# Performance work log

Measured on AMD Instinct MI355X. Metric: run time of the kernel, lower is better.

Reference implementation:

```python
import jax, jax.numpy as jnp
import numpy as np

B, T, N, D = 2, 16, 512, 256
HID, HEADS = 256, 8
HD = HID // HEADS // 2  # 16
SCALE = HD ** -0.5
LAMBDA_INIT = 0.8 - 0.6 * float(np.exp(-0.3 * (2 - 1)))  # layer_idx = 2
LN_EPS = 1e-5


def setup_inputs() -> dict:
    key = jax.random.key(0)
    ks = jax.random.split(key, 8)
    return {
        "x": jax.random.normal(ks[0], (B, T, N, D), dtype=jnp.float32),
        "Wq": jax.random.normal(ks[1], (D, HID), dtype=jnp.float32) * (D ** -0.5),
        "Wk": jax.random.normal(ks[2], (D, HID), dtype=jnp.float32) * (D ** -0.5),
        "Wv": jax.random.normal(ks[3], (D, HID), dtype=jnp.float32) * (D ** -0.5),
        "lq1": jax.random.normal(ks[4], (HD,), dtype=jnp.float32) * 0.1,
        "lk1": jax.random.normal(ks[5], (HD,), dtype=jnp.float32) * 0.1,
        "lq2": jax.random.normal(ks[6], (HD,), dtype=jnp.float32) * 0.1,
        "lk2": jax.random.normal(ks[7], (HD,), dtype=jnp.float32) * 0.1,
        "ln_gamma": jnp.ones((2 * HD,), dtype=jnp.float32),
        "ln_beta": jnp.zeros((2 * HD,), dtype=jnp.float32),
    }


def _attn_pair(q, k, v1, v2):
    # q,k,v*: [BT, N, H, HD]; shared softmax applied to both value halves
    p = jax.nn.softmax(jnp.einsum('bnhd,bmhd->bhnm', q, k) * SCALE, axis=-1)
    o1 = jnp.einsum('bhnm,bmhd->bnhd', p, v1)
    o2 = jnp.einsum('bhnm,bmhd->bnhd', p, v2)
    return jnp.concatenate([o1, o2], axis=-1)  # [BT, N, H, 2*HD]


def reference(x, Wq, Wk, Wv, lq1, lk1, lq2, lk2, ln_gamma, ln_beta):
    b, t, n, d = x.shape
    # 1x1 Conv2d over channel dim == per-token linear projection
    q = jnp.einsum('btnd,dh->btnh', x, Wq).reshape(b * t, n, HEADS, 2 * HD)
    k = jnp.einsum('btnd,dh->btnh', x, Wk).reshape(b * t, n, HEADS, 2 * HD)
    v = jnp.einsum('btnd,dh->btnh', x, Wv).reshape(b * t, n, HEADS, 2 * HD)
    q1, q2 = jnp.split(q, 2, axis=-1)
    k1, k2 = jnp.split(k, 2, axis=-1)
    v1, v2 = jnp.split(v, 2, axis=-1)
    attn1 = _attn_pair(q1, k1, v1, v2)
    attn2 = _attn_pair(q2, k2, v1, v2)
    lam = jnp.exp(jnp.sum(lq1 * lk1)) - jnp.exp(jnp.sum(lq2 * lk2)) + LAMBDA_INIT
    y = attn1 - lam * attn2  # [BT, N, H, 2*HD]
    mu = jnp.mean(y, axis=-1, keepdims=True)
    var = jnp.mean(jnp.square(y - mu), axis=-1, keepdims=True)
    y = (y - mu) * jax.lax.rsqrt(var + LN_EPS) * ln_gamma + ln_beta
    y = y * (1.0 - LAMBDA_INIT)
    return y.reshape(b, t, n, HEADS * 2 * HD)
```

## Files before the change

kernel.cpp:

```cpp
#include <hip/hip_runtime.h>
#include <cmath>

typedef unsigned short u16;
typedef unsigned int   u32;
typedef __attribute__((ext_vector_type(8)))  short short8;
typedef __attribute__((ext_vector_type(4)))  float f32x4;
typedef __attribute__((ext_vector_type(16))) float f32x16;

constexpr int BT    = 32;
constexpr int NTOK  = 512;
constexpr int DIM   = 256;
constexpr int HID   = 256;
constexpr int M_ROWS = BT * NTOK;
constexpr int HM     = M_ROWS * 32;
constexpr size_t TENS = (size_t)M_ROWS * HID;
constexpr float LAMBDA_INIT  = 0.35550906759096927f;
constexpr float ONE_MINUS_LI = 0.6444909324090307f;
constexpr float LN_EPS = 1e-5f;
constexpr float QSCALE = 0.36067376022224085f;

#define MFMA16(a, b, c) __builtin_amdgcn_mfma_f32_16x16x32_bf16((a), (b), (c), 0, 0, 0)
#define MFMA32(a, b, c) __builtin_amdgcn_mfma_f32_32x32x16_bf16((a), (b), (c), 0, 0, 0)

__device__ __forceinline__ u16 f2bf(float f) {
    u32 u = __float_as_uint(f);
    return (u16)((u + 0x7FFFu + ((u >> 16) & 1u)) >> 16);
}

__device__ __forceinline__ float fexp2(float x) {
#if defined(__has_builtin) && __has_builtin(__builtin_amdgcn_exp2f)
    return __builtin_amdgcn_exp2f(x);
#else
    return exp2f(x);
#endif
}

__device__ __forceinline__ u32 pack_trunc(float a, float b) {
    return __builtin_amdgcn_perm(__float_as_uint(b), __float_as_uint(a), 0x07060302u);
}

__global__ __launch_bounds__(256) void prep_w(const float* __restrict__ Wq,
                                              const float* __restrict__ Wk,
                                              const float* __restrict__ Wv,
                                              u16* __restrict__ Wt) {
    const float* W = (blockIdx.z == 0) ? Wq : (blockIdx.z == 1) ? Wk : Wv;
    u16* dst = Wt + (size_t)blockIdx.z * 65536;
    __shared__ float T[64][65];
    const int k0 = blockIdx.x * 64, n0 = blockIdx.y * 64;
    const int tr = threadIdx.x >> 4;
    const int tc = threadIdx.x & 15;
    #pragma unroll
    for (int i = 0; i < 4; ++i) {
        int row = tr + i * 16;
        float4 v = *(const float4*)&W[(size_t)(k0 + row) * HID + n0 + tc * 4];
        T[row][tc * 4 + 0] = v.x; T[row][tc * 4 + 1] = v.y;
        T[row][tc * 4 + 2] = v.z; T[row][tc * 4 + 3] = v.w;
    }
    __syncthreads();
    #pragma unroll
    for (int i = 0; i < 4; ++i) {
        int n = tr + i * 16;
        int k4 = tc * 4;
        uint2 pk;
        pk.x = (u32)f2bf(T[k4 + 0][n]) | ((u32)f2bf(T[k4 + 1][n]) << 16);
        pk.y = (u32)f2bf(T[k4 + 2][n]) | ((u32)f2bf(T[k4 + 3][n]) << 16);
        *(uint2*)&dst[(size_t)(n0 + n) * DIM + k0 + k4] = pk;
    }
}

__global__ __launch_bounds__(256, 3) void proj_kernel(
    const float* __restrict__ x, const u16* __restrict__ Wt,
    u16* __restrict__ Qh, u16* __restrict__ Kh, u16* __restrict__ Vh)
{
    __shared__ u16 As[64 * 72];
    __shared__ u16 Bs[3][64 * 72];

    const int tid  = threadIdx.x;
    const int n0   = blockIdx.x * 64;
    const int m0   = blockIdx.y * 64;
    const int lane = tid & 63;
    const int wv   = tid >> 6;
    const int q16  = lane & 15;
    const int quad = lane >> 4;
    const int mw   = (wv >> 1) * 32;
    const int nw   = (wv & 1) * 32;

    const int sr = tid >> 2;
    const int sc = (tid & 3) * 16;

    f32x4 acc[3][4];
    #pragma unroll
    for (int z = 0; z < 3; ++z)
        #pragma unroll
        for (int t = 0; t < 4; ++t)
            acc[z][t] = (f32x4){0.f, 0.f, 0.f, 0.f};

    float4 ga[4];
    uint4  gb[3][2];
    {
        const float4* xs = (const float4*)&x[(size_t)(m0 + sr) * DIM + sc];
        ga[0] = xs[0]; ga[1] = xs[1]; ga[2] = xs[2]; ga[3] = xs[3];
        #pragma unroll
        for (int z = 0; z < 3; ++z) {
            const uint4* ws4 = (const uint4*)&Wt[(size_t)z * 65536 + (size_t)(n0 + sr) * DIM + sc];
            gb[z][0] = ws4[0]; gb[z][1] = ws4[1];
        }
    }

    for (int it = 0; it < 4; ++it) {
        {
            uint4 o0, o1;
            o0.x = (u32)f2bf(ga[0].x) | ((u32)f2bf(ga[0].y) << 16);
            o0.y = (u32)f2bf(ga[0].z) | ((u32)f2bf(ga[0].w) << 16);
            o0.z = (u32)f2bf(ga[1].x) | ((u32)f2bf(ga[1].y) << 16);
            o0.w = (u32)f2bf(ga[1].z) | ((u32)f2bf(ga[1].w) << 16);
            o1.x = (u32)f2bf(ga[2].x) | ((u32)f2bf(ga[2].y) << 16);
            o1.y = (u32)f2bf(ga[2].z) | ((u32)f2bf(ga[2].w) << 16);
            o1.z = (u32)f2bf(ga[3].x) | ((u32)f2bf(ga[3].y) << 16);
            o1.w = (u32)f2bf(ga[3].z) | ((u32)f2bf(ga[3].w) << 16);
            *(uint4*)&As[sr * 72 + sc]     = o0;
            *(uint4*)&As[sr * 72 + sc + 8] = o1;
            #pragma unroll
            for (int z = 0; z < 3; ++z) {
                *(uint4*)&Bs[z][sr * 72 + sc]     = gb[z][0];
                *(uint4*)&Bs[z][sr * 72 + sc + 8] = gb[z][1];
            }
        }
        __syncthreads();

        if (it < 3) {
            const int kk = (it + 1) * 64;
            const float4* xs = (const float4*)&x[(size_t)(m0 + sr) * DIM + kk + sc];
            ga[0] = xs[0]; ga[1] = xs[1]; ga[2] = xs[2]; ga[3] = xs[3];
            #pragma unroll
            for (int z = 0; z < 3; ++z) {
                const uint4* ws4 = (const uint4*)&Wt[(size_t)z * 65536 + (size_t)(n0 + sr) * DIM + kk + sc];
                gb[z][0] = ws4[0]; gb[z][1] = ws4[1];
            }
        }

        #pragma unroll
        for (int kc = 0; kc < 2; ++kc) {
            short8 a0 = *(const short8*)&As[(mw +      q16) * 72 + kc * 32 + quad * 8];
            short8 a1 = *(const short8*)&As[(mw + 16 + q16) * 72 + kc * 32 + quad * 8];
            #pragma unroll
            for (int z = 0; z < 3; ++z) {
                short8 b0 = *(const short8*)&Bs[z][(nw +      q16) * 72 + kc * 32 + quad * 8];
                short8 b1 = *(const short8*)&Bs[z][(nw + 16 + q16) * 72 + kc * 32 + quad * 8];
                acc[z][0] = MFMA16(a0, b0, acc[z][0]);
                acc[z][1] = MFMA16(a0, b1, acc[z][1]);
                acc[z][2] = MFMA16(a1, b0, acc[z][2]);
                acc[z][3] = MFMA16(a1, b1, acc[z][3]);
            }
        }
        __syncthreads();
    }

    const int hcol = (n0 + nw) >> 5;
    #pragma unroll
    for (int z = 0; z < 3; ++z) {
        u16* C = (z == 0) ? Qh : (z == 1) ? Kh : Vh;
        u16* base = C + (size_t)hcol * HM;
        const float s = (z == 0) ? QSCALE : 1.0f;
        #pragma unroll
        for (int r = 0; r < 4; ++r) {
            const int row = m0 + mw + quad * 4 + r;
            base[(size_t)row * 32 + q16]              = f2bf(acc[z][0][r] * s);
            base[(size_t)row * 32 + q16 + 16]         = f2bf(acc[z][1][r] * s);
            base[(size_t)(row + 16) * 32 + q16]       = f2bf(acc[z][2][r] * s);
            base[(size_t)(row + 16) * 32 + q16 + 16]  = f2bf(acc[z][3][r] * s);
        }
    }
}

__global__ __launch_bounds__(256, 3) void attn_kernel(
    const u16* __restrict__ Qh, const u16* __restrict__ Kh, const u16* __restrict__ Vh,
    const float* __restrict__ lq1, const float* __restrict__ lk1,
    const float* __restrict__ lq2, const float* __restrict__ lk2,
    const float* __restrict__ gamma, const float* __restrict__ beta,
    float* __restrict__ out)
{
    __shared__ u16 Ks[256 * 40];
    __shared__ u16 Vts[32 * 264];
    __shared__ u16 Pb[4][32 * 40];

    const int qh  = blockIdx.x;
    const int h   = blockIdx.y;
    const int bt  = blockIdx.z;
    const int tid = threadIdx.x;
    const int lane = tid & 63;
    const int wv   = tid >> 6;
    const int l31  = lane & 31;
    const int hi   = lane >> 5;

    float sa = 0.f, sb = 0.f;
    #pragma unroll
    for (int d = 0; d < 16; ++d) { sa += lq1[d] * lk1[d]; sb += lq2[d] * lk2[d]; }
    const float lam = __expf(sa) - __expf(sb) + LAMBDA_INIT;

    const int qbase = bt * NTOK + qh * 128 + wv * 32;
    const u16* qrowp = Qh + (size_t)h * HM + (size_t)(qbase + l31) * 32 + hi * 8;
    const short8 B1 = *(const short8*)qrowp;
    const short8 B2 = *(const short8*)(qrowp + 16);

    const f32x16 z16 = {0.f,0.f,0.f,0.f,0.f,0.f,0.f,0.f,0.f,0.f,0.f,0.f,0.f,0.f,0.f,0.f};
    f32x16 O1 = z16, O2 = z16;
    float l1 = 0.f, l2 = 0.f;
    u16* P = &Pb[wv][0];

    for (int chunk = 0; chunk < 2; ++chunk) {
        if (chunk) __syncthreads();
        {
            const uint4* src = (const uint4*)(Kh + (size_t)h * HM +
                                (size_t)(bt * NTOK + chunk * 256 + tid) * 32);
            uint4* dst = (uint4*)&Ks[tid * 40];
            dst[0] = src[0]; dst[1] = src[1]; dst[2] = src[2]; dst[3] = src[3];
        }
        if (tid < 128) {
            const int j0 = tid * 2;
            const u16* v0 = Vh + (size_t)h * HM + (size_t)(bt * NTOK + chunk * 256 + j0) * 32;
            union U { uint4 q[4]; u32 w[16]; } ra, rb;
            #pragma unroll
            for (int i = 0; i < 4; ++i) {
                ra.q[i] = ((const uint4*)v0)[i];
                rb.q[i] = ((const uint4*)(v0 + 32))[i];
            }
            #pragma unroll
            for (int w = 0; w < 16; ++w) {
                u32 lo = __builtin_amdgcn_perm(rb.w[w], ra.w[w], 0x05040100u);
                u32 hi2 = __builtin_amdgcn_perm(rb.w[w], ra.w[w], 0x07060302u);
                *(u32*)&Vts[(2 * w)     * 264 + j0] = lo;
                *(u32*)&Vts[(2 * w + 1) * 264 + j0] = hi2;
            }
        }
        __syncthreads();

        for (int kc = 0; kc < 8; ++kc) {
            const u16* krow = &Ks[(kc * 32 + l31) * 40 + hi * 8];
            const short8 A1 = *(const short8*)krow;
            const short8 A2 = *(const short8*)(krow + 16);
            const u16* vrow = &Vts[l31 * 264 + kc * 32 + hi * 8];
            const short8 Vt0 = *(const short8*)vrow;
            const short8 Vt1 = *(const short8*)(vrow + 16);

            f32x16 S = MFMA32(A1, B1, z16);
            #pragma unroll
            for (int rg = 0; rg < 4; ++rg) {
                float e0 = fexp2(S[4 * rg + 0]);
                float e1 = fexp2(S[4 * rg + 1]);
                float e2 = fexp2(S[4 * rg + 2]);
                float e3 = fexp2(S[4 * rg + 3]);
                l1 += (e0 + e1) + (e2 + e3);
                uint2 w; w.x = pack_trunc(e0, e1); w.y = pack_trunc(e2, e3);
                *(uint2*)&P[l31 * 40 + rg * 8 + hi * 4] = w;
            }
            {
                const short8 P0  = *(const short8*)&P[l31 * 40 + hi * 8];
                const short8 P1f = *(const short8*)&P[l31 * 40 + 16 + hi * 8];
                O1 = MFMA32(P0,  Vt0, O1);
                O1 = MFMA32(P1f, Vt1, O1);
            }
            S = MFMA32(A2, B2, z16);
            #pragma unroll
            for (int rg = 0; rg < 4; ++rg) {
                float e0 = fexp2(S[4 * rg + 0]);
                float e1 = fexp2(S[4 * rg + 1]);
                float e2 = fexp2(S[4 * rg + 2]);
                float e3 = fexp2(S[4 * rg + 3]);
                l2 += (e0 + e1) + (e2 + e3);
                uint2 w; w.x = pack_trunc(e0, e1); w.y = pack_trunc(e2, e3);
                *(uint2*)&P[l31 * 40 + rg * 8 + hi * 4] = w;
            }
            {
                const short8 P0  = *(const short8*)&P[l31 * 40 + hi * 8];
                const short8 P1f = *(const short8*)&P[l31 * 40 + 16 + hi * 8];
                O2 = MFMA32(P0,  Vt0, O2);
                O2 = MFMA32(P1f, Vt1, O2);
            }
        }
    }

    l1 += __shfl_xor(l1, 32);
    l2 += __shfl_xor(l2, 32);
    const float i1base = 1.0f / l1;
    const float i2base = 1.0f / l2;
    const float g = gamma[l31];
    const float bc = beta[l31];

    #pragma unroll
    for (int r = 0; r < 16; ++r) {
        const int qloc = (r & 3) + 8 * (r >> 2) + 4 * hi;
        const float i1 = __shfl(i1base, qloc);
        const float i2 = __shfl(i2base, qloc);
        float y = O1[r] * i1 - lam * (O2[r] * i2);

        float s  = y;
        float s2 = y * y;
        #pragma unroll
        for (int off = 1; off < 32; off <<= 1) {
            s  += __shfl_xor(s,  off);
            s2 += __shfl_xor(s2, off);
        }
        const float mu   = s * (1.0f / 32.0f);
        const float var  = s2 * (1.0f / 32.0f) - mu * mu;
        const float rstd = rsqrtf(var + LN_EPS);

        const int row = qbase + qloc;
        out[(size_t)row * HID + h * 32 + l31] = ((y - mu) * rstd * g + bc) * ONE_MINUS_LI;
    }
}

extern "C" void kernel_launch(void* const* d_in, const int* in_sizes, int n_in,
                              void* d_out, int out_size, void* d_ws, size_t ws_size,
                              hipStream_t stream) {
    const float* x   = (const float*)d_in[0];
    const float* Wq  = (const float*)d_in[1];
    const float* Wk  = (const float*)d_in[2];
    const float* Wv  = (const float*)d_in[3];
    const float* lq1 = (const float*)d_in[4];
    const float* lk1 = (const float*)d_in[5];
    const float* lq2 = (const float*)d_in[6];
    const float* lk2 = (const float*)d_in[7];
    const float* gam = (const float*)d_in[8];
    const float* bet = (const float*)d_in[9];
    float* out = (float*)d_out;

    u16* ws = (u16*)d_ws;
    u16* Wt = ws;
    u16* Qh = Wt + 3 * 65536;
    u16* Kh = Qh + TENS;
    u16* Vh = Kh + TENS;

    hipLaunchKernelGGL(prep_w, dim3(4, 4, 3), dim3(256), 0, stream, Wq, Wk, Wv, Wt);
    hipLaunchKernelGGL(proj_kernel, dim3(HID / 64, M_ROWS / 64), dim3(256), 0, stream,
                       x, Wt, Qh, Kh, Vh);
    hipLaunchKernelGGL(attn_kernel, dim3(4, 8, 32), dim3(256), 0, stream,
                       Qh, Kh, Vh, lq1, lk1, lq2, lk2, gam, bet, out);
}
```

Before: 157.4 us.

## Interleave dual-softmax MFMAs, re-pad LDS, and vectorize projection stores

The attention inner loop now issues both QK^T MFMAs up front and writes both probability tiles into separate per-wave LDS buffers, so exp work on one half can overlap the other half's matrix ops. K and P LDS rows are re-padded from 40 to 36 elements and read with paired 64-bit loads to change the bank-conflict pattern. The projection kernel swaps its MFMA operands so each lane holds four consecutive output columns, which lets it write packed 8-byte stores instead of scattered 2-byte ones. Occupancy for the projection kernel is raised to 4 blocks per SM, which adds register pressure, and the doubled P buffer increases LDS use.

```diff
diff --git a/kernel.cpp b/kernel.cpp
--- a/kernel.cpp
+++ b/kernel.cpp
@@ -39,6 +39,14 @@
     return __builtin_amdgcn_perm(__float_as_uint(b), __float_as_uint(a), 0x07060302u);
 }
 
+__device__ __forceinline__ short8 ldb64x2(const u16* p) {
+    uint2 a = *(const uint2*)p;
+    uint2 b = *(const uint2*)(p + 4);
+    union { u32 u[4]; short8 s; } x;
+    x.u[0] = a.x; x.u[1] = a.y; x.u[2] = b.x; x.u[3] = b.y;
+    return x.s;
+}
+
 __global__ __launch_bounds__(256) void prep_w(const float* __restrict__ Wq,
                                               const float* __restrict__ Wk,
                                               const float* __restrict__ Wv,
@@ -68,7 +76,7 @@
     }
 }
 
-__global__ __launch_bounds__(256, 3) void proj_kernel(
+__global__ __launch_bounds__(256, 4) void proj_kernel(
     const float* __restrict__ x, const u16* __restrict__ Wt,
     u16* __restrict__ Qh, u16* __restrict__ Kh, u16* __restrict__ Vh)
 {
@@ -147,10 +155,10 @@
             for (int z = 0; z < 3; ++z) {
                 short8 b0 = *(const short8*)&Bs[z][(nw +      q16) * 72 + kc * 32 + quad * 8];
                 short8 b1 = *(const short8*)&Bs[z][(nw + 16 + q16) * 72 + kc * 32 + quad * 8];
-                acc[z][0] = MFMA16(a0, b0, acc[z][0]);
-                acc[z][1] = MFMA16(a0, b1, acc[z][1]);
-                acc[z][2] = MFMA16(a1, b0, acc[z][2]);
-                acc[z][3] = MFMA16(a1, b1, acc[z][3]);
+                acc[z][0] = MFMA16(b0, a0, acc[z][0]);
+                acc[z][1] = MFMA16(b1, a0, acc[z][1]);
+                acc[z][2] = MFMA16(b0, a1, acc[z][2]);
+                acc[z][3] = MFMA16(b1, a1, acc[z][3]);
             }
         }
         __syncthreads();
@@ -163,12 +171,13 @@
         u16* base = C + (size_t)hcol * HM;
         const float s = (z == 0) ? QSCALE : 1.0f;
         #pragma unroll
-        for (int r = 0; r < 4; ++r) {
-            const int row = m0 + mw + quad * 4 + r;
-            base[(size_t)row * 32 + q16]              = f2bf(acc[z][0][r] * s);
-            base[(size_t)row * 32 + q16 + 16]         = f2bf(acc[z][1][r] * s);
-            base[(size_t)(row + 16) * 32 + q16]       = f2bf(acc[z][2][r] * s);
-            base[(size_t)(row + 16) * 32 + q16 + 16]  = f2bf(acc[z][3][r] * s);
+        for (int t = 0; t < 4; ++t) {
+            const int m  = m0 + mw + ((t >> 1) << 4) + q16;
+            const int c0 = ((t & 1) << 4) + quad * 4;
+            uint2 w;
+            w.x = (u32)f2bf(acc[z][t][0] * s) | ((u32)f2bf(acc[z][t][1] * s) << 16);
+            w.y = (u32)f2bf(acc[z][t][2] * s) | ((u32)f2bf(acc[z][t][3] * s) << 16);
+            *(uint2*)&base[(size_t)m * 32 + c0] = w;
         }
     }
 }
@@ -180,9 +189,9 @@
     const float* __restrict__ gamma, const float* __restrict__ beta,
     float* __restrict__ out)
 {
-    __shared__ u16 Ks[256 * 40];
+    __shared__ u16 Ks[256 * 36];
     __shared__ u16 Vts[32 * 264];
-    __shared__ u16 Pb[4][32 * 40];
+    __shared__ u16 Pb[4][2][32 * 36];
 
     const int qh  = blockIdx.x;
     const int h   = blockIdx.y;
@@ -206,15 +215,19 @@
     const f32x16 z16 = {0.f,0.f,0.f,0.f,0.f,0.f,0.f,0.f,0.f,0.f,0.f,0.f,0.f,0.f,0.f,0.f};
     f32x16 O1 = z16, O2 = z16;
     float l1 = 0.f, l2 = 0.f;
-    u16* P = &Pb[wv][0];
+    u16* P1 = &Pb[wv][0][0];
+    u16* P2 = &Pb[wv][1][0];
 
     for (int chunk = 0; chunk < 2; ++chunk) {
         if (chunk) __syncthreads();
         {
             const uint4* src = (const uint4*)(Kh + (size_t)h * HM +
                                 (size_t)(bt * NTOK + chunk * 256 + tid) * 32);
-            uint4* dst = (uint4*)&Ks[tid * 40];
-            dst[0] = src[0]; dst[1] = src[1]; dst[2] = src[2]; dst[3] = src[3];
+            union { uint4 q[4]; uint2 d[8]; } kb;
+            kb.q[0] = src[0]; kb.q[1] = src[1]; kb.q[2] = src[2]; kb.q[3] = src[3];
+            uint2* dst = (uint2*)&Ks[tid * 36];
+            #pragma unroll
+            for (int i = 0; i < 8; ++i) dst[i] = kb.d[i];
         }
         if (tid < 128) {
             const int j0 = tid * 2;
@@ -227,7 +240,7 @@
             }
             #pragma unroll
             for (int w = 0; w < 16; ++w) {
-                u32 lo = __builtin_amdgcn_perm(rb.w[w], ra.w[w], 0x05040100u);
+                u32 lo  = __builtin_amdgcn_perm(rb.w[w], ra.w[w], 0x05040100u);
                 u32 hi2 = __builtin_amdgcn_perm(rb.w[w], ra.w[w], 0x07060302u);
                 *(u32*)&Vts[(2 * w)     * 264 + j0] = lo;
                 *(u32*)&Vts[(2 * w + 1) * 264 + j0] = hi2;
@@ -236,46 +249,44 @@
         __syncthreads();
 
         for (int kc = 0; kc < 8; ++kc) {
-            const u16* krow = &Ks[(kc * 32 + l31) * 40 + hi * 8];
-            const short8 A1 = *(const short8*)krow;
-            const short8 A2 = *(const short8*)(krow + 16);
+            const u16* krow = &Ks[(kc * 32 + l31) * 36];
+            const short8 A1 = ldb64x2(krow + hi * 8);
+            const short8 A2 = ldb64x2(krow + 16 + hi * 8);
             const u16* vrow = &Vts[l31 * 264 + kc * 32 + hi * 8];
             const short8 Vt0 = *(const short8*)vrow;
             const short8 Vt1 = *(const short8*)(vrow + 16);
 
-            f32x16 S = MFMA32(A1, B1, z16);
+            f32x16 S1 = MFMA32(A1, B1, z16);
+            f32x16 S2 = MFMA32(A2, B2, z16);
             #pragma unroll
             for (int rg = 0; rg < 4; ++rg) {
-                float e0 = fexp2(S[4 * rg + 0]);
-                float e1 = fexp2(S[4 * rg + 1]);
-                float e2 = fexp2(S[4 * rg + 2]);
-                float e3 = fexp2(S[4 * rg + 3]);
+                float e0 = fexp2(S1[4 * rg + 0]);
+                float e1 = fexp2(S1[4 * rg + 1]);
+                float e2 = fexp2(S1[4 * rg + 2]);
+                float e3 = fexp2(S1[4 * rg + 3]);
                 l1 += (e0 + e1) + (e2 + e3);
                 uint2 w; w.x = pack_trunc(e0, e1); w.y = pack_trunc(e2, e3);
-                *(uint2*)&P[l31 * 40 + rg * 8 + hi * 4] = w;
-            }
-            {
-                const short8 P0  = *(const short8*)&P[l31 * 40 + hi * 8];
-                const short8 P1f = *(const short8*)&P[l31 * 40 + 16 + hi * 8];
-                O1 = MFMA32(P0,  Vt0, O1);
-                O1 = MFMA32(P1f, Vt1, O1);
-            }
-            S = MFMA32(A2, B2, z16);
+                *(uint2*)&P1[l31 * 36 + rg * 8 + hi * 4] = w;
+            }
             #pragma unroll
             for (int rg = 0; rg < 4; ++rg) {
-                float e0 = fexp2(S[4 * rg + 0]);
-                float e1 = fexp2(S[4 * rg + 1]);
-                float e2 = fexp2(S[4 * rg + 2]);
-                float e3 = fexp2(S[4 * rg + 3]);
+                float e0 = fexp2(S2[4 * rg + 0]);
+                float e1 = fexp2(S2[4 * rg + 1]);
+                float e2 = fexp2(S2[4 * rg + 2]);
+                float e3 = fexp2(S2[4 * rg + 3]);
                 l2 += (e0 + e1) + (e2 + e3);
                 uint2 w; w.x = pack_trunc(e0, e1); w.y = pack_trunc(e2, e3);
-                *(uint2*)&P[l31 * 40 + rg * 8 + hi * 4] = w;
+                *(uint2*)&P2[l31 * 36 + rg * 8 + hi * 4] = w;
             }
             {
-                const short8 P0  = *(const short8*)&P[l31 * 40 + hi * 8];
-                const short8 P1f = *(const short8*)&P[l31 * 40 + 16 + hi * 8];
-                O2 = MFMA32(P0,  Vt0, O2);
-                O2 = MFMA32(P1f, Vt1, O2);
+                const short8 Pa0 = ldb64x2(&P1[l31 * 36 + hi * 8]);
+                const short8 Pa1 = ldb64x2(&P1[l31 * 36 + 16 + hi * 8]);
+                const short8 Pb0 = ldb64x2(&P2[l31 * 36 + hi * 8]);
+                const short8 Pb1 = ldb64x2(&P2[l31 * 36 + 16 + hi * 8]);
+                O1 = MFMA32(Pa0, Vt0, O1);
+                O1 = MFMA32(Pa1, Vt1, O1);
+                O2 = MFMA32(Pb0, Vt0, O2);
+                O2 = MFMA32(Pb1, Vt1, O2);
             }
         }
     }
@@ -284,7 +295,7 @@
     l2 += __shfl_xor(l2, 32);
     const float i1base = 1.0f / l1;
     const float i2base = 1.0f / l2;
-    const float g = gamma[l31];
+    const float g  = gamma[l31];
     const float bc = beta[l31];
 
     #pragma unroll
```

Result: no change. 159.8 us (+1.6%).
